# Optimization experiments

Measured on AMD Instinct MI355X. Metric: run time of the kernel, lower is better.

## Reference

```python
import jax, jax.numpy as jnp
import numpy as np

HEADS = 8

def conv1x1(x, w):
    # x: [B,I,H,W], w: [O,I,1,1] (torch Conv2d layout)
    return jnp.einsum('bihw,oi->bohw', x, w[:, :, 0, 0])

def dwconv3(x, w):
    # depthwise 3x3, w: [C,1,3,3]
    return jax.lax.conv_general_dilated(
        x, w, (1, 1), ((1, 1), (1, 1)),
        feature_group_count=x.shape[1],
        dimension_numbers=('NCHW', 'OIHW', 'NCHW'))

def ln_ch(x, w, b):
    # LayerNorm over channel dim of [B,C,H,W] (equiv. to nn.LayerNorm on 'b (h w) c')
    mu = jnp.mean(x, axis=1, keepdims=True)
    xc = x - mu
    var = jnp.mean(xc * xc, axis=1, keepdims=True)
    return (xc / jnp.sqrt(var + 1e-5)) * w[None, :, None, None] + b[None, :, None, None]

def l2norm(x):
    # F.normalize(dim=-1), eps=1e-12
    n = jnp.sqrt(jnp.sum(x * x, axis=-1, keepdims=True))
    return x / jnp.maximum(n, 1e-12)

def attn_block(qmap, fmap, temp, qw, qdw, kvw, kvdw, pw):
    # Restormer-style transposed (channel) attention
    q = dwconv3(conv1x1(qmap, qw), qdw)
    kv = dwconv3(conv1x1(fmap, kvw), kvdw)
    k, v = jnp.split(kv, 2, axis=1)
    B, C, H, W = q.shape
    c = C // HEADS
    q = l2norm(q.reshape(B, HEADS, c, H * W))
    k = l2norm(k.reshape(B, HEADS, c, H * W))
    v = v.reshape(B, HEADS, c, H * W)
    attn = jax.nn.softmax(jnp.einsum('bhcn,bhdn->bhcd', q, k) * temp, axis=-1)
    out = jnp.einsum('bhcd,bhdn->bhcn', attn, v).reshape(B, C, H, W)
    return conv1x1(out, pw)

def ffn_block(x, inw, dww, outw):
    # gated dwconv FFN: gelu(x1) * x2
    x1, x2 = jnp.split(dwconv3(conv1x1(x, inw), dww), 2, axis=1)
    return conv1x1(jax.nn.gelu(x1, approximate=False) * x2, outw)

def setup_inputs():
    key = jax.random.key(0)
    B, C, H, W, N = 16, 96, 64, 64, 3
    D = C * N
    ks = jax.random.split(key, 32)
    rn = lambda k, s: jax.random.normal(k, s, dtype=jnp.float32) * 0.02
    return {
        'q_L': jax.random.normal(ks[0], (B, C, H, W), jnp.float32),
        'q_H': jax.random.normal(ks[1], (B, C, N, H, W), jnp.float32),
        'fuse_L': jax.random.normal(ks[2], (B, C, H, W), jnp.float32),
        'fuse_H': jax.random.normal(ks[3], (B, C, N, H, W), jnp.float32),
        'n1_w': jnp.ones((C,), jnp.float32), 'n1_b': jnp.zeros((C,), jnp.float32),
        'n2_w': jnp.ones((C,), jnp.float32), 'n2_b': jnp.zeros((C,), jnp.float32),
        'n3_w': jnp.ones((D,), jnp.float32), 'n3_b': jnp.zeros((D,), jnp.float32),
        'n4_w': jnp.ones((D,), jnp.float32), 'n4_b': jnp.zeros((D,), jnp.float32),
        'a1_temp': jnp.ones((HEADS, 1, 1), jnp.float32),
        'a1_q': rn(ks[4], (C, C, 1, 1)), 'a1_qdw': rn(ks[5], (C, 1, 3, 3)),
        'a1_kv': rn(ks[6], (2 * C, C, 1, 1)), 'a1_kvdw': rn(ks[7], (2 * C, 1, 3, 3)),
        'a1_po': rn(ks[8], (C, C, 1, 1)),
        'f1_in': rn(ks[9], (4 * C, C, 1, 1)), 'f1_dw': rn(ks[10], (4 * C, 1, 3, 3)),
        'f1_out': rn(ks[11], (C, 2 * C, 1, 1)),
        'a2_temp': jnp.ones((HEADS, 1, 1), jnp.float32),
        'a2_q': rn(ks[12], (D, D, 1, 1)), 'a2_qdw': rn(ks[13], (D, 1, 3, 3)),
        'a2_kv': rn(ks[14], (2 * D, D, 1, 1)), 'a2_kvdw': rn(ks[15], (2 * D, 1, 3, 3)),
        'a2_po': rn(ks[16], (D, D, 1, 1)),
        'f2_in': rn(ks[17], (4 * D, D, 1, 1)), 'f2_dw': rn(ks[18], (4 * D, 1, 3, 3)),
        'f2_out': rn(ks[19], (D, 2 * D, 1, 1)),
    }

def reference(q_L, q_H, fuse_L, fuse_H,
              n1_w, n1_b, n2_w, n2_b, n3_w, n3_b, n4_w, n4_b,
              a1_temp, a1_q, a1_qdw, a1_kv, a1_kvdw, a1_po,
              f1_in, f1_dw, f1_out,
              a2_temp, a2_q, a2_qdw, a2_kv, a2_kvdw, a2_po,
              f2_in, f2_dw, f2_out):
    B, C, H, W = q_L.shape
    N = q_H.shape[2]
    qH = q_H.reshape(B, C * N, H, W)   # 'b c n h w -> b (c n) h w'
    fH = fuse_H.reshape(B, C * N, H, W)
    x = q_L + attn_block(ln_ch(q_L, n1_w, n1_b), fuse_L,
                         a1_temp, a1_q, a1_qdw, a1_kv, a1_kvdw, a1_po)
    x = x + ffn_block(ln_ch(x, n2_w, n2_b), f1_in, f1_dw, f1_out)
    y = qH + attn_block(ln_ch(qH, n3_w, n3_b), fH,
                        a2_temp, a2_q, a2_qdw, a2_kv, a2_kvdw, a2_po)
    y = y + ffn_block(ln_ch(y, n4_w, n4_b), f2_in, f2_dw, f2_out)
    return x, y.reshape(B, C, N, H, W)  # (q_L, (q_H,))
```

## Files before the change

### kernel.cpp

```cpp
#include <hip/hip_runtime.h>
#include <math.h>

#define HWS 4096
#define BATCH 16
#define WDIM 64

typedef _Float16 half8 __attribute__((ext_vector_type(8)));
typedef _Float16 half4 __attribute__((ext_vector_type(4)));
typedef _Float16 half2v __attribute__((ext_vector_type(2)));
typedef float floatx4 __attribute__((ext_vector_type(4)));

__global__ void wcvt_kernel(const float* __restrict__ src, _Float16* __restrict__ dst, int n) {
  int i = blockIdx.x * 256 + threadIdx.x;
  if (i < n) dst[i] = (_Float16)src[i];
}

__global__ void ln16_kernel(const float* __restrict__ x, const float* __restrict__ w,
                            const float* __restrict__ bia, _Float16* __restrict__ out, int CH) {
  int b = blockIdx.y;
  int p = blockIdx.x * blockDim.x + threadIdx.x;
  const float* xp = x + (size_t)b * CH * HWS + p;
  float s = 0.f, s2 = 0.f;
  for (int c = 0; c < CH; ++c) { float v = xp[(size_t)c * HWS]; s += v; s2 = fmaf(v, v, s2); }
  float mu = s / CH;
  float var = s2 / CH - mu * mu;
  float inv = rsqrtf(var + 1e-5f);
  _Float16* op = out + ((size_t)b * HWS + p) * CH;
  for (int c = 0; c < CH; c += 4) {
    half4 hv;
    #pragma unroll
    for (int j = 0; j < 4; ++j) {
      float v = (xp[(size_t)(c + j) * HWS] - mu) * inv * w[c + j] + bia[c + j];
      hv[j] = (_Float16)v;
    }
    *reinterpret_cast<half4*>(&op[c]) = hv;
  }
}

__global__ void xcvt16_kernel(const float* __restrict__ x, _Float16* __restrict__ out, int CH) {
  int b = blockIdx.y;
  int p = blockIdx.x * blockDim.x + threadIdx.x;
  const float* xp = x + (size_t)b * CH * HWS + p;
  _Float16* op = out + ((size_t)b * HWS + p) * CH;
  for (int c = 0; c < CH; c += 4) {
    half4 hv;
    #pragma unroll
    for (int j = 0; j < 4; ++j) hv[j] = (_Float16)xp[(size_t)(c + j) * HWS];
    *reinterpret_cast<half4*>(&op[c]) = hv;
  }
}

template<bool RES>
__launch_bounds__(256)
__global__ void conv1x1_mfma(const _Float16* __restrict__ X16, const _Float16* __restrict__ W16,
                             const float* __restrict__ res, float* __restrict__ out,
                             int I, int O) {
  __shared__ _Float16 Xs[256 * 56];
  int b = blockIdx.z;
  int o0 = blockIdx.y * 96;
  int p0 = blockIdx.x * 256;
  int tid = threadIdx.x;
  int lane = tid & 63;
  int wn0 = (tid >> 6) * 64;
  int l15 = lane & 15, kg = lane >> 4;
  const _Float16* Xb = X16 + ((size_t)b * HWS + p0) * I;
  floatx4 acc[6][4] = {};
  int spl = tid >> 2, skc = (tid & 3) * 8;
  for (int k0 = 0; k0 < I; k0 += 32) {
    #pragma unroll
    for (int it = 0; it < 4; ++it) {
      half8 v = *reinterpret_cast<const half8*>(&Xb[(size_t)(spl + it * 64) * I + k0 + skc]);
      *reinterpret_cast<half8*>(&Xs[(spl + it * 64) * 56 + skc]) = v;
    }
    __syncthreads();
    half8 af[6], bf[4];
    #pragma unroll
    for (int mi = 0; mi < 6; ++mi)
      af[mi] = *reinterpret_cast<const half8*>(&W16[(size_t)(o0 + mi * 16 + l15) * I + k0 + kg * 8]);
    #pragma unroll
    for (int ni = 0; ni < 4; ++ni)
      bf[ni] = *reinterpret_cast<const half8*>(&Xs[(wn0 + ni * 16 + l15) * 56 + kg * 8]);
    #pragma unroll
    for (int mi = 0; mi < 6; ++mi)
      #pragma unroll
      for (int ni = 0; ni < 4; ++ni)
        acc[mi][ni] = __builtin_amdgcn_mfma_f32_16x16x32_f16(af[mi], bf[ni], acc[mi][ni], 0, 0, 0);
    __syncthreads();
  }
  int r4 = kg * 4;
  #pragma unroll
  for (int mi = 0; mi < 6; ++mi) {
    #pragma unroll
    for (int v = 0; v < 4; ++v) {
      int o = o0 + mi * 16 + r4 + v;
      size_t rowb = ((size_t)b * O + o) * HWS + p0;
      #pragma unroll
      for (int ni = 0; ni < 4; ++ni) {
        int p = wn0 + ni * 16 + l15;
        float val = acc[mi][ni][v];
        if (RES) val += res[rowb + p];
        out[rowb + p] = val;
      }
    }
  }
}

__global__ void dw3_kernel(const float* __restrict__ in, const float* __restrict__ w,
                           float* __restrict__ out, int CH) {
  int bc = blockIdx.y;
  int ch = bc % CH;
  int p = blockIdx.x * blockDim.x + threadIdx.x;
  int y = p >> 6, x = p & 63;
  const float* ip = in + (size_t)bc * HWS;
  const float* wp = w + ch * 9;
  float s = 0.f;
  #pragma unroll
  for (int ky = 0; ky < 3; ++ky) {
    int yy = y + ky - 1;
    if (yy < 0 || yy >= WDIM) continue;
    #pragma unroll
    for (int kx = 0; kx < 3; ++kx) {
      int xx = x + kx - 1;
      if (xx < 0 || xx >= WDIM) continue;
      s = fmaf(wp[ky * 3 + kx], ip[yy * WDIM + xx], s);
    }
  }
  out[(size_t)bc * HWS + p] = s;
}

__global__ void rownorm_kernel(const float* __restrict__ src, float* __restrict__ dst,
                               int CH, int ROWMUL) {
  int bc = blockIdx.x;
  int b = bc / CH, ch = bc % CH;
  const float* p = src + ((size_t)b * ROWMUL + ch) * HWS;
  float s = 0.f;
  for (int i = threadIdx.x; i < HWS; i += 256) { float v = p[i]; s = fmaf(v, v, s); }
  #pragma unroll
  for (int off = 32; off > 0; off >>= 1) s += __shfl_down(s, off, 64);
  __shared__ float red[4];
  int lane = threadIdx.x & 63, wv = threadIdx.x >> 6;
  if (lane == 0) red[wv] = s;
  __syncthreads();
  if (threadIdx.x == 0) {
    float t = red[0] + red[1] + red[2] + red[3];
    dst[bc] = fmaxf(sqrtf(t), 1e-12f);
  }
}

template<int c>
__global__ void qk_partial_kernel(const float* __restrict__ qb, const float* __restrict__ kvb,
                                  float* __restrict__ part, int CH) {
  constexpr int TC = c / 4;
  int split = blockIdx.x, bh = blockIdx.y;
  int b = bh >> 3, h = bh & 7;
  const float* qrow = qb + ((size_t)b * CH + h * c) * HWS;
  const float* krow = kvb + ((size_t)b * 2 * CH + h * c) * HWS;
  __shared__ float qs[c][65];
  __shared__ float ks[c][65];
  int tid = threadIdx.x;
  int tc = tid / TC, td = tid % TC;
  bool active = tid < TC * TC;
  float acc[4][4] = {};
  for (int s = 0; s < 8; ++s) {
    int n0 = split * 512 + s * 64;
    for (int e = tid; e < c * 64; e += 128) {
      int r = e >> 6, col = e & 63;
      qs[r][col] = qrow[(size_t)r * HWS + n0 + col];
      ks[r][col] = krow[(size_t)r * HWS + n0 + col];
    }
    __syncthreads();
    if (active) {
      for (int kk = 0; kk < 64; ++kk) {
        float a[4], bb[4];
        #pragma unroll
        for (int i = 0; i < 4; ++i) { a[i] = qs[tc * 4 + i][kk]; bb[i] = ks[td * 4 + i][kk]; }
        #pragma unroll
        for (int i = 0; i < 4; ++i)
          #pragma unroll
          for (int j = 0; j < 4; ++j)
            acc[i][j] = fmaf(a[i], bb[j], acc[i][j]);
      }
    }
    __syncthreads();
  }
  if (active) {
    #pragma unroll
    for (int i = 0; i < 4; ++i)
      #pragma unroll
      for (int j = 0; j < 4; ++j)
        part[(((size_t)bh * 8 + split) * 36 + tc * 4 + i) * 36 + td * 4 + j] = acc[i][j];
  }
}

template<int c>
__global__ void attn_softmax_kernel(const float* __restrict__ part, const float* __restrict__ nq,
                                    const float* __restrict__ nk, const float* __restrict__ temp,
                                    float* __restrict__ attnw, int CH) {
  int bh = blockIdx.x;
  int b = bh >> 3, h = bh & 7;
  __shared__ float Ss[c][c];
  int tid = threadIdx.x;
  for (int e = tid; e < c * c; e += 64) {
    int r = e / c, d = e % c;
    float s = 0.f;
    for (int sp = 0; sp < 8; ++sp)
      s += part[(((size_t)bh * 8 + sp) * 36 + r) * 36 + d];
    s = s / (nq[b * CH + h * c + r] * nk[b * CH + h * c + d]) * temp[h];
    Ss[r][d] = s;
  }
  __syncthreads();
  if (tid < c) {
    int r = tid;
    float m = -1e30f;
    for (int d = 0; d < c; ++d) m = fmaxf(m, Ss[r][d]);
    float sum = 0.f;
    for (int d = 0; d < c; ++d) { float e = expf(Ss[r][d] - m); sum += e; Ss[r][d] = e; }
    float inv = 1.f / sum;
    for (int d = 0; d < c; ++d)
      attnw[((size_t)bh * 36 + r) * 36 + d] = Ss[r][d] * inv;
  }
}

template<int c>
__global__ void pv_kernel(const float* __restrict__ attnw, const float* __restrict__ kvb,
                          _Float16* __restrict__ out, int CH) {
  __shared__ float As[c * c];
  int p = blockIdx.x * blockDim.x + threadIdx.x;
  int h = blockIdx.y, b = blockIdx.z;
  int bh = b * 8 + h;
  for (int e = threadIdx.x; e < c * c; e += 256)
    As[e] = attnw[((size_t)bh * 36 + e / c) * 36 + e % c];
  __syncthreads();
  const float* vb = kvb + ((size_t)b * 2 * CH + CH + h * c) * HWS + p;
  float vr[c];
  #pragma unroll
  for (int d = 0; d < c; ++d) vr[d] = vb[(size_t)d * HWS];
  _Float16* ob = out + ((size_t)b * HWS + p) * CH + h * c;
  #pragma unroll
  for (int ci = 0; ci < c; ci += 2) {
    float s0 = 0.f, s1 = 0.f;
    #pragma unroll
    for (int d = 0; d < c; ++d) {
      s0 = fmaf(As[ci * c + d], vr[d], s0);
      s1 = fmaf(As[(ci + 1) * c + d], vr[d], s1);
    }
    half2v hv; hv[0] = (_Float16)s0; hv[1] = (_Float16)s1;
    *reinterpret_cast<half2v*>(&ob[ci]) = hv;
  }
}

__global__ void dwgate16_kernel(const float* __restrict__ in, const float* __restrict__ w,
                                _Float16* __restrict__ out, int C2) {
  int b = blockIdx.z;
  int ch0 = blockIdx.y * 32;
  int p = blockIdx.x * 256 + threadIdx.x;
  int y = p >> 6, x = p & 63;
  const float* base = in + (size_t)b * 2 * C2 * HWS;
  _Float16* ob = out + ((size_t)b * HWS + p) * C2 + ch0;
  for (int c8 = 0; c8 < 32; c8 += 8) {
    half8 hv;
    #pragma unroll
    for (int chl = 0; chl < 8; ++chl) {
      int ch = ch0 + c8 + chl;
      const float* i1 = base + (size_t)ch * HWS;
      const float* i2 = base + (size_t)(ch + C2) * HWS;
      const float* w1 = w + ch * 9;
      const float* w2 = w + (ch + C2) * 9;
      float s1 = 0.f, s2 = 0.f;
      #pragma unroll
      for (int ky = 0; ky < 3; ++ky) {
        int yy = y + ky - 1;
        if (yy < 0 || yy >= WDIM) continue;
        #pragma unroll
        for (int kx = 0; kx < 3; ++kx) {
          int xx = x + kx - 1;
          if (xx < 0 || xx >= WDIM) continue;
          s1 = fmaf(w1[ky * 3 + kx], i1[yy * WDIM + xx], s1);
          s2 = fmaf(w2[ky * 3 + kx], i2[yy * WDIM + xx], s2);
        }
      }
      float g = 0.5f * s1 * (1.f + erff(s1 * 0.70710678118654752f));
      hv[chl] = (_Float16)(g * s2);
    }
    *reinterpret_cast<half8*>(&ob[c8]) = hv;
  }
}

template<int c>
static void run_branch(const float* xin, const float* fmap,
                       const float* n1w, const float* n1b, const float* n2w, const float* n2b,
                       const float* temp, const _Float16* qw16, const float* qdw,
                       const _Float16* kvw16, const float* kvdw, const _Float16* pw16,
                       const _Float16* finw16, const float* fdw, const _Float16* foutw16,
                       float* xout, float* ws, size_t U, int NB, hipStream_t stream) {
  const int CH = 8 * c;
  float* U0 = ws;
  float* U1 = ws + U;
  float* U2 = ws + 2 * U;
  float* U3 = ws + 3 * U;
  float* U4 = ws + 4 * U;
  float* U5 = ws + 5 * U;
  float* part  = ws + 6 * U;
  float* attnw = part + (size_t)NB * 82944;
  float* nq    = attnw + (size_t)NB * 10368;
  float* nk    = nq + (size_t)NB * 288;

  dim3 blk(256);
  ln16_kernel<<<dim3(16, NB), blk, 0, stream>>>(xin, n1w, n1b, (_Float16*)U0, CH);
  conv1x1_mfma<false><<<dim3(16, CH / 96, NB), blk, 0, stream>>>((_Float16*)U0, qw16, nullptr, U1, CH, CH);
  dw3_kernel<<<dim3(16, NB * CH), blk, 0, stream>>>(U1, qdw, U2, CH);
  xcvt16_kernel<<<dim3(16, NB), blk, 0, stream>>>(fmap, (_Float16*)U5, CH);
  conv1x1_mfma<false><<<dim3(16, 2 * CH / 96, NB), blk, 0, stream>>>((_Float16*)U5, kvw16, nullptr, U3, CH, 2 * CH);
  dw3_kernel<<<dim3(16, NB * 2 * CH), blk, 0, stream>>>(U3, kvdw, U0, 2 * CH);
  rownorm_kernel<<<dim3(NB * CH), blk, 0, stream>>>(U2, nq, CH, CH);
  rownorm_kernel<<<dim3(NB * CH), blk, 0, stream>>>(U0, nk, CH, 2 * CH);
  qk_partial_kernel<c><<<dim3(8, NB * 8), dim3(128), 0, stream>>>(U2, U0, part, CH);
  attn_softmax_kernel<c><<<dim3(NB * 8), dim3(64), 0, stream>>>(part, nq, nk, temp, attnw, CH);
  pv_kernel<c><<<dim3(16, 8, NB), blk, 0, stream>>>(attnw, U0, (_Float16*)U3, CH);
  conv1x1_mfma<true><<<dim3(16, CH / 96, NB), blk, 0, stream>>>((_Float16*)U3, pw16, xin, xout, CH, CH);
  ln16_kernel<<<dim3(16, NB), blk, 0, stream>>>(xout, n2w, n2b, (_Float16*)U5, CH);
  conv1x1_mfma<false><<<dim3(16, 4 * CH / 96, NB), blk, 0, stream>>>((_Float16*)U5, finw16, nullptr, U0, CH, 4 * CH);
  dwgate16_kernel<<<dim3(16, 2 * CH / 32, NB), blk, 0, stream>>>(U0, fdw, (_Float16*)U4, 2 * CH);
  conv1x1_mfma<true><<<dim3(16, CH / 96, NB), blk, 0, stream>>>((_Float16*)U4, foutw16, xout, xout, 2 * CH, CH);
}

extern "C" void kernel_launch(void* const* d_in, const int* in_sizes, int n_in,
                              void* d_out, int out_size, void* d_ws, size_t ws_size,
                              hipStream_t stream) {
  const float* q_L    = (const float*)d_in[0];
  const float* q_H    = (const float*)d_in[1];
  const float* fuse_L = (const float*)d_in[2];
  const float* fuse_H = (const float*)d_in[3];
  const float* n1_w = (const float*)d_in[4];
  const float* n1_b = (const float*)d_in[5];
  const float* n2_w = (const float*)d_in[6];
  const float* n2_b = (const float*)d_in[7];
  const float* n3_w = (const float*)d_in[8];
  const float* n3_b = (const float*)d_in[9];
  const float* n4_w = (const float*)d_in[10];
  const float* n4_b = (const float*)d_in[11];
  const float* a1_temp = (const float*)d_in[12];
  const float* a1_q    = (const float*)d_in[13];
  const float* a1_qdw  = (const float*)d_in[14];
  const float* a1_kv   = (const float*)d_in[15];
  const float* a1_kvdw = (const float*)d_in[16];
  const float* a1_po   = (const float*)d_in[17];
  const float* f1_in   = (const float*)d_in[18];
  const float* f1_dw   = (const float*)d_in[19];
  const float* f1_out  = (const float*)d_in[20];
  const float* a2_temp = (const float*)d_in[21];
  const float* a2_q    = (const float*)d_in[22];
  const float* a2_qdw  = (const float*)d_in[23];
  const float* a2_kv   = (const float*)d_in[24];
  const float* a2_kvdw = (const float*)d_in[25];
  const float* a2_po   = (const float*)d_in[26];
  const float* f2_in   = (const float*)d_in[27];
  const float* f2_dw   = (const float*)d_in[28];
  const float* f2_out  = (const float*)d_in[29];

  float* out = (float*)d_out;
  float* ws  = (float*)d_ws;

  const size_t W16TOT = 921600;
  int NB = 16;
  while (NB > 1) {
    size_t U = (size_t)NB * 288 * HWS;
    size_t smallf = (size_t)NB * (82944 + 10368 + 288 + 288);
    size_t need = (6 * U + smallf) * sizeof(float) + W16TOT * sizeof(_Float16);
    if (need <= ws_size) break;
    NB >>= 1;
  }
  size_t U = (size_t)NB * 288 * HWS;
  size_t smallf = (size_t)NB * (82944 + 10368 + 288 + 288);
  _Float16* w16 = (_Float16*)(ws + 6 * U + smallf);

  const float* wsrc[10] = {a1_q, a1_kv, a1_po, f1_in, f1_out, a2_q, a2_kv, a2_po, f2_in, f2_out};
  const int    wcnt[10] = {9216, 18432, 9216, 36864, 18432, 82944, 165888, 82944, 331776, 165888};
  _Float16* wptr[10];
  {
    size_t off = 0;
    for (int i = 0; i < 10; ++i) {
      wptr[i] = w16 + off;
      wcvt_kernel<<<dim3((wcnt[i] + 255) / 256), dim3(256), 0, stream>>>(wsrc[i], wptr[i], wcnt[i]);
      off += wcnt[i];
    }
  }

  for (int b0 = 0; b0 < BATCH; b0 += NB) {
    run_branch<12>(q_L + (size_t)b0 * 96 * HWS, fuse_L + (size_t)b0 * 96 * HWS,
                   n1_w, n1_b, n2_w, n2_b, a1_temp,
                   wptr[0], a1_qdw, wptr[1], a1_kvdw, wptr[2],
                   wptr[3], f1_dw, wptr[4],
                   out + (size_t)b0 * 96 * HWS, ws, U, NB, stream);
  }
  float* out2 = out + (size_t)BATCH * 96 * HWS;
  for (int b0 = 0; b0 < BATCH; b0 += NB) {
    run_branch<36>(q_H + (size_t)b0 * 288 * HWS, fuse_H + (size_t)b0 * 288 * HWS,
                   n3_w, n3_b, n4_w, n4_b, a2_temp,
                   wptr[5], a2_qdw, wptr[6], a2_kvdw, wptr[7],
                   wptr[8], f2_dw, wptr[9],
                   out2 + (size_t)b0 * 288 * HWS, ws, U, NB, stream);
  }
}
```

Before: 2.802 ms.

## Stage transposed fp16 stores through LDS and fuse row norms into dwconv

The kernels that write channel-last fp16 tensors (layernorm, conversion, pv, gated dwconv) now stage each tile in shared memory and write it back as contiguous vector stores, replacing strided per-pixel stores. The separate rownorm kernels are removed. The depthwise conv now reduces squared outputs per block and atomically adds them into a zeroed buffer, and a small kernel then takes sqrt and max. This drops a full re-read of the q and k tensors, at the cost of extra barriers, shared memory use, atomic traffic and nondeterministic summation order.

```diff
diff --git a/kernel.cpp b/kernel.cpp
--- a/kernel.cpp
+++ b/kernel.cpp
@@ -7,7 +7,6 @@
 
 typedef _Float16 half8 __attribute__((ext_vector_type(8)));
 typedef _Float16 half4 __attribute__((ext_vector_type(4)));
-typedef _Float16 half2v __attribute__((ext_vector_type(2)));
 typedef float floatx4 __attribute__((ext_vector_type(4)));
 
 __global__ void wcvt_kernel(const float* __restrict__ src, _Float16* __restrict__ dst, int n) {
@@ -15,38 +14,77 @@
   if (i < n) dst[i] = (_Float16)src[i];
 }
 
+__global__ void zero_kernel(float* __restrict__ p, int n) {
+  int i = blockIdx.x * 256 + threadIdx.x;
+  if (i < n) p[i] = 0.f;
+}
+
+__global__ void sqrtmax_kernel(float* __restrict__ p, int n) {
+  int i = blockIdx.x * 256 + threadIdx.x;
+  if (i < n) p[i] = fmaxf(sqrtf(p[i]), 1e-12f);
+}
+
 __global__ void ln16_kernel(const float* __restrict__ x, const float* __restrict__ w,
                             const float* __restrict__ bia, _Float16* __restrict__ out, int CH) {
+  __shared__ _Float16 T[256][38];
   int b = blockIdx.y;
-  int p = blockIdx.x * blockDim.x + threadIdx.x;
+  int tid = threadIdx.x;
+  int p = blockIdx.x * 256 + tid;
   const float* xp = x + (size_t)b * CH * HWS + p;
   float s = 0.f, s2 = 0.f;
   for (int c = 0; c < CH; ++c) { float v = xp[(size_t)c * HWS]; s += v; s2 = fmaf(v, v, s2); }
   float mu = s / CH;
   float var = s2 / CH - mu * mu;
   float inv = rsqrtf(var + 1e-5f);
-  _Float16* op = out + ((size_t)b * HWS + p) * CH;
-  for (int c = 0; c < CH; c += 4) {
-    half4 hv;
-    #pragma unroll
-    for (int j = 0; j < 4; ++j) {
-      float v = (xp[(size_t)(c + j) * HWS] - mu) * inv * w[c + j] + bia[c + j];
-      hv[j] = (_Float16)v;
-    }
-    *reinterpret_cast<half4*>(&op[c]) = hv;
+  _Float16* ob = out + ((size_t)b * HWS + (size_t)blockIdx.x * 256) * CH;
+  for (int c0 = 0; c0 < CH; c0 += 32) {
+    #pragma unroll
+    for (int c8 = 0; c8 < 32; c8 += 8) {
+      half8 hv;
+      #pragma unroll
+      for (int j = 0; j < 8; ++j) {
+        int c = c0 + c8 + j;
+        float v = (xp[(size_t)c * HWS] - mu) * inv * w[c] + bia[c];
+        hv[j] = (_Float16)v;
+      }
+      *reinterpret_cast<half8*>(&T[tid][c8]) = hv;
+    }
+    __syncthreads();
+    #pragma unroll
+    for (int it = 0; it < 4; ++it) {
+      int f = it * 256 + tid;
+      int px = f >> 2, co = (f & 3) * 8;
+      half8 v = *reinterpret_cast<const half8*>(&T[px][co]);
+      *reinterpret_cast<half8*>(&ob[(size_t)px * CH + c0 + co]) = v;
+    }
+    __syncthreads();
   }
 }
 
 __global__ void xcvt16_kernel(const float* __restrict__ x, _Float16* __restrict__ out, int CH) {
+  __shared__ _Float16 T[256][38];
   int b = blockIdx.y;
-  int p = blockIdx.x * blockDim.x + threadIdx.x;
+  int tid = threadIdx.x;
+  int p = blockIdx.x * 256 + tid;
   const float* xp = x + (size_t)b * CH * HWS + p;
-  _Float16* op = out + ((size_t)b * HWS + p) * CH;
-  for (int c = 0; c < CH; c += 4) {
-    half4 hv;
-    #pragma unroll
-    for (int j = 0; j < 4; ++j) hv[j] = (_Float16)xp[(size_t)(c + j) * HWS];
-    *reinterpret_cast<half4*>(&op[c]) = hv;
+  _Float16* ob = out + ((size_t)b * HWS + (size_t)blockIdx.x * 256) * CH;
+  for (int c0 = 0; c0 < CH; c0 += 32) {
+    #pragma unroll
+    for (int c8 = 0; c8 < 32; c8 += 8) {
+      half8 hv;
+      #pragma unroll
+      for (int j = 0; j < 8; ++j) hv[j] = (_Float16)xp[(size_t)(c0 + c8 + j) * HWS];
+      *reinterpret_cast<half8*>(&T[tid][c8]) = hv;
+    }
+    __syncthreads();
+    #pragma unroll
+    for (int it = 0; it < 4; ++it) {
+      int f = it * 256 + tid;
+      int px = f >> 2, co = (f & 3) * 8;
+      half8 v = *reinterpret_cast<const half8*>(&T[px][co]);
+      *reinterpret_cast<half8*>(&ob[(size_t)px * CH + c0 + co]) = v;
+    }
+    __syncthreads();
   }
 }
 
@@ -106,9 +144,10 @@
 }
 
 __global__ void dw3_kernel(const float* __restrict__ in, const float* __restrict__ w,
-                           float* __restrict__ out, int CH) {
+                           float* __restrict__ out, int CH,
+                           float* __restrict__ sumsq, int normCH) {
   int bc = blockIdx.y;
-  int ch = bc % CH;
+  int b = bc / CH, ch = bc % CH;
   int p = blockIdx.x * blockDim.x + threadIdx.x;
   int y = p >> 6, x = p & 63;
   const float* ip = in + (size_t)bc * HWS;
@@ -126,24 +165,16 @@
     }
   }
   out[(size_t)bc * HWS + p] = s;
-}
-
-__global__ void rownorm_kernel(const float* __restrict__ src, float* __restrict__ dst,
-                               int CH, int ROWMUL) {
-  int bc = blockIdx.x;
-  int b = bc / CH, ch = bc % CH;
-  const float* p = src + ((size_t)b * ROWMUL + ch) * HWS;
-  float s = 0.f;
-  for (int i = threadIdx.x; i < HWS; i += 256) { float v = p[i]; s = fmaf(v, v, s); }
-  #pragma unroll
-  for (int off = 32; off > 0; off >>= 1) s += __shfl_down(s, off, 64);
+  float v = (ch < normCH) ? s * s : 0.f;
+  #pragma unroll
+  for (int off = 32; off > 0; off >>= 1) v += __shfl_down(v, off, 64);
   __shared__ float red[4];
   int lane = threadIdx.x & 63, wv = threadIdx.x >> 6;
-  if (lane == 0) red[wv] = s;
+  if (lane == 0) red[wv] = v;
   __syncthreads();
-  if (threadIdx.x == 0) {
+  if (threadIdx.x == 0 && ch < normCH) {
     float t = red[0] + red[1] + red[2] + red[3];
-    dst[bc] = fmaxf(sqrtf(t), 1e-12f);
+    atomicAdd(&sumsq[b * normCH + ch], t);
   }
 }
 
@@ -224,39 +255,53 @@
 template<int c>
 __global__ void pv_kernel(const float* __restrict__ attnw, const float* __restrict__ kvb,
                           _Float16* __restrict__ out, int CH) {
+  constexpr int CPAD = (c == 36) ? 38 : 14;
+  constexpr int Q4 = c / 4;
   __shared__ float As[c * c];
-  int p = blockIdx.x * blockDim.x + threadIdx.x;
+  __shared__ _Float16 T[256][CPAD];
+  int tid = threadIdx.x;
+  int p = blockIdx.x * 256 + tid;
   int h = blockIdx.y, b = blockIdx.z;
   int bh = b * 8 + h;
-  for (int e = threadIdx.x; e < c * c; e += 256)
+  for (int e = tid; e < c * c; e += 256)
     As[e] = attnw[((size_t)bh * 36 + e / c) * 36 + e % c];
   __syncthreads();
   const float* vb = kvb + ((size_t)b * 2 * CH + CH + h * c) * HWS + p;
   float vr[c];
   #pragma unroll
   for (int d = 0; d < c; ++d) vr[d] = vb[(size_t)d * HWS];
-  _Float16* ob = out + ((size_t)b * HWS + p) * CH + h * c;
-  #pragma unroll
-  for (int ci = 0; ci < c; ci += 2) {
-    float s0 = 0.f, s1 = 0.f;
-    #pragma unroll
-    for (int d = 0; d < c; ++d) {
-      s0 = fmaf(As[ci * c + d], vr[d], s0);
-      s1 = fmaf(As[(ci + 1) * c + d], vr[d], s1);
-    }
-    half2v hv; hv[0] = (_Float16)s0; hv[1] = (_Float16)s1;
-    *reinterpret_cast<half2v*>(&ob[ci]) = hv;
+  #pragma unroll
+  for (int ci = 0; ci < c; ci += 4) {
+    half4 hv;
+    #pragma unroll
+    for (int j = 0; j < 4; ++j) {
+      float s = 0.f;
+      #pragma unroll
+      for (int d = 0; d < c; ++d) s = fmaf(As[(ci + j) * c + d], vr[d], s);
+      hv[j] = (_Float16)s;
+    }
+    *reinterpret_cast<half4*>(&T[tid][ci]) = hv;
+  }
+  __syncthreads();
+  _Float16* ob = out + ((size_t)b * HWS + (size_t)blockIdx.x * 256) * CH + h * c;
+  #pragma unroll
+  for (int it = 0; it < Q4; ++it) {
+    int f = it * 256 + tid;
+    int px = f / Q4, co = (f % Q4) * 4;
+    half4 v = *reinterpret_cast<const half4*>(&T[px][co]);
+    *reinterpret_cast<half4*>(&ob[(size_t)px * CH + co]) = v;
   }
 }
 
 __global__ void dwgate16_kernel(const float* __restrict__ in, const float* __restrict__ w,
                                 _Float16* __restrict__ out, int C2) {
+  __shared__ _Float16 T[256][38];
   int b = blockIdx.z;
   int ch0 = blockIdx.y * 32;
-  int p = blockIdx.x * 256 + threadIdx.x;
+  int tid = threadIdx.x;
+  int p = blockIdx.x * 256 + tid;
   int y = p >> 6, x = p & 63;
   const float* base = in + (size_t)b * 2 * C2 * HWS;
-  _Float16* ob = out + ((size_t)b * HWS + p) * C2 + ch0;
   for (int c8 = 0; c8 < 32; c8 += 8) {
     half8 hv;
     #pragma unroll
@@ -282,7 +327,16 @@
       float g = 0.5f * s1 * (1.f + erff(s1 * 0.70710678118654752f));
       hv[chl] = (_Float16)(g * s2);
     }
-    *reinterpret_cast<half8*>(&ob[c8]) = hv;
+    *reinterpret_cast<half8*>(&T[tid][c8]) = hv;
+  }
+  __syncthreads();
+  _Float16* ob = out + ((size_t)b * HWS + (size_t)blockIdx.x * 256) * C2 + ch0;
+  #pragma unroll
+  for (int it = 0; it < 4; ++it) {
+    int f = it * 256 + tid;
+    int px = f >> 2, co = (f & 3) * 8;
+    half8 v = *reinterpret_cast<const half8*>(&T[px][co]);
+    *reinterpret_cast<half8*>(&ob[(size_t)px * C2 + co]) = v;
   }
 }
 
@@ -306,14 +360,15 @@
   float* nk    = nq + (size_t)NB * 288;
 
   dim3 blk(256);
+  int nrm = 2 * NB * 288;
   ln16_kernel<<<dim3(16, NB), blk, 0, stream>>>(xin, n1w, n1b, (_Float16*)U0, CH);
+  zero_kernel<<<dim3((nrm + 255) / 256), blk, 0, stream>>>(nq, nrm);
   conv1x1_mfma<false><<<dim3(16, CH / 96, NB), blk, 0, stream>>>((_Float16*)U0, qw16, nullptr, U1, CH, CH);
-  dw3_kernel<<<dim3(16, NB * CH), blk, 0, stream>>>(U1, qdw, U2, CH);
+  dw3_kernel<<<dim3(16, NB * CH), blk, 0, stream>>>(U1, qdw, U2, CH, nq, CH);
   xcvt16_kernel<<<dim3(16, NB), blk, 0, stream>>>(fmap, (_Float16*)U5, CH);
   conv1x1_mfma<false><<<dim3(16, 2 * CH / 96, NB), blk, 0, stream>>>((_Float16*)U5, kvw16, nullptr, U3, CH, 2 * CH);
-  dw3_kernel<<<dim3(16, NB * 2 * CH), blk, 0, stream>>>(U3, kvdw, U0, 2 * CH);
-  rownorm_kernel<<<dim3(NB * CH), blk, 0, stream>>>(U2, nq, CH, CH);
-  rownorm_kernel<<<dim3(NB * CH), blk, 0, stream>>>(U0, nk, CH, 2 * CH);
+  dw3_kernel<<<dim3(16, NB * 2 * CH), blk, 0, stream>>>(U3, kvdw, U0, 2 * CH, nk, CH);
+  sqrtmax_kernel<<<dim3((nrm + 255) / 256), blk, 0, stream>>>(nq, nrm);
   qk_partial_kernel<c><<<dim3(8, NB * 8), dim3(128), 0, stream>>>(U2, U0, part, CH);
   attn_softmax_kernel<c><<<dim3(NB * 8), dim3(64), 0, stream>>>(part, nq, nk, temp, attnw, CH);
   pv_kernel<c><<<dim3(16, 8, NB), blk, 0, stream>>>(attnw, U0, (_Float16*)U3, CH);
```

After: 2.721 ms. 1.03x faster.
